# Performance work log

Measured on AMD Instinct MI355X. Metric: run time of the kernel, lower is better.

The kernel has to match this reference:

```python
import jax, jax.numpy as jnp
import numpy as np

FEAT = 128   # feat_dim == hidden_size
EDGE = 128   # edge_dim
H = FEAT
D = FEAT + EDGE          # TimeLSTM input size (att_dim)
SCALE = 5000000.0        # newAmazon time-decay divisor
B, L = 2048, 200


def setup_inputs() -> dict:
    key = jax.random.key(0)
    ks = jax.random.split(key, 12)
    seq = jax.random.normal(ks[0], (B, L, FEAT), jnp.float32)
    seq_e = jax.random.normal(ks[1], (B, L, EDGE), jnp.float32)
    # descending timestamps so time_span >= 0 (matches the module's assert)
    td = jax.random.randint(ks[2], (B, L), 0, 10_000_000)
    time_diff = jnp.flip(jnp.sort(td, axis=1), axis=1).astype(jnp.float32)
    src = jax.random.normal(ks[3], (B, FEAT), jnp.float32)
    src_t = jax.random.normal(ks[4], (B,), jnp.float32)
    seq_t = jax.random.normal(ks[5], (B, L), jnp.float32)
    mask = jnp.zeros((B, L), dtype=jnp.bool_)

    def lin(k, out_d, in_d):
        return (jax.random.normal(k, (out_d, in_d), jnp.float32)
                * np.float32(1.0 / np.sqrt(in_d)))

    # TimeLSTM params (W_all: h->4h, U_all: input->4h, W_d: h->h)
    W_all, b_W = lin(ks[6], 4 * H, H), jnp.zeros((4 * H,), jnp.float32)
    U_all, b_U = lin(ks[7], 4 * H, D), jnp.zeros((4 * H,), jnp.float32)
    W_d, b_d = lin(ks[8], H, H), jnp.zeros((H,), jnp.float32)
    # MergeLayer params
    fc1_w, fc1_b = lin(ks[9], FEAT, 2 * FEAT), jnp.zeros((FEAT,), jnp.float32)
    fc2_w, fc2_b = lin(ks[10], FEAT, FEAT), jnp.zeros((FEAT,), jnp.float32)
    return dict(src=src, src_t=src_t, seq=seq, seq_t=seq_t, seq_e=seq_e,
                time_diff=time_diff, mask=mask,
                W_all=W_all, b_W=b_W, U_all=U_all, b_U=b_U,
                W_d=W_d, b_d=b_d,
                fc1_w=fc1_w, fc1_b=fc1_b, fc2_w=fc2_w, fc2_b=fc2_b)


def reference(src, src_t, seq, seq_t, seq_e, time_diff, mask,
              W_all, b_W, U_all, b_U, W_d, b_d,
              fc1_w, fc1_b, fc2_w, fc2_b):
    # src_t, seq_t, mask are accepted but unused, matching the torch forward.
    seq_x = jnp.concatenate([seq, seq_e], axis=2)              # [B, L, D]
    # vectorized version of the python time-decay loop:
    # time_span[:, j] = (time_diff[:, j-1] - time_diff[:, j]) / SCALE, span[:,0]=0
    span = (time_diff[:, :-1] - time_diff[:, 1:]) / SCALE      # [B, L-1]
    time_span = jnp.concatenate(
        [jnp.zeros_like(time_diff[:, :1]), span], axis=1)      # [B, L]

    # batch the input projection over all timesteps in one GEMM
    u = jnp.einsum('bld,gd->blg', seq_x, U_all) + b_U          # [B, L, 4H]

    h0 = jnp.zeros((seq_x.shape[0], H), seq_x.dtype)
    c0 = jnp.zeros_like(h0)

    def step(carry, xs):
        h, c = carry
        u_t, t_t = xs                                          # [B,4H], [B]
        c_s1 = jnp.tanh(c @ W_d.T + b_d)                       # short-term mem
        c_adj = c - c_s1 + c_s1 * t_t[:, None]                 # time-decayed cell
        gates = h @ W_all.T + b_W + u_t
        f, i, o, g = jnp.split(gates, 4, axis=1)
        f = jax.nn.sigmoid(f)
        i = jax.nn.sigmoid(i)
        o = jax.nn.sigmoid(o)
        g = jax.nn.sigmoid(g)   # note: repo TimeLSTM uses sigmoid, not tanh
        c_new = f * c_adj + i * g
        h_new = o * jnp.tanh(c_new)
        return (h_new, c_new), h_new

    (hn, _cn), _outs = jax.lax.scan(
        step, (h0, c0), (jnp.swapaxes(u, 0, 1), time_span.T))  # scan over L

    # MergeLayer: fc2(relu(fc1(cat([hn, src]))))
    x = jnp.concatenate([hn, src], axis=1)                     # [B, 2*FEAT]
    hmid = jax.nn.relu(x @ fc1_w.T + fc1_b)
    return hmid @ fc2_w.T + fc2_b                              # [B, FEAT]
```

## Files before the change

kernel.cpp:

```cpp
#include <hip/hip_runtime.h>
#include <hip/hip_bf16.h>
#include <stdint.h>

#define L_ 200
#define SCALE_ 5000000.0f

typedef __attribute__((ext_vector_type(8))) short bf16x8;
typedef __attribute__((ext_vector_type(4))) float f32x4;

static __device__ __forceinline__ short to_bf16(float f) {
    __hip_bfloat16 h = __float2bfloat16(f);
    return *reinterpret_cast<short*>(&h);
}
static __device__ __forceinline__ float fsig(float x) {
    return __builtin_amdgcn_rcpf(1.0f + __builtin_amdgcn_exp2f(-1.442695041f * x));
}
static __device__ __forceinline__ float ftanh(float x) {
    return 1.0f - 2.0f * __builtin_amdgcn_rcpf(1.0f + __builtin_amdgcn_exp2f(2.885390082f * x));
}
static __device__ __forceinline__ float bf_lo(unsigned p) {
    union { unsigned u; float f; } c; c.u = p << 16; return c.f;
}
static __device__ __forceinline__ float bf_hi(unsigned p) {
    union { unsigned u; float f; } c; c.u = p & 0xffff0000u; return c.f;
}

__global__ void prep_kernel(const float* __restrict__ U_all, const float* __restrict__ W_all,
                            const float* __restrict__ W_d, const float* __restrict__ b_W,
                            const float* __restrict__ b_U, const float* __restrict__ b_d,
                            const float* __restrict__ time_diff,
                            short* __restrict__ ufrag, short* __restrict__ wfrag,
                            short* __restrict__ wdfrag, float* __restrict__ bias512,
                            float* __restrict__ bdo, float* __restrict__ tsw,
                            int n_total) {
    int i = blockIdx.x * 256 + threadIdx.x;
    if (i >= n_total) return;
    if (i < 131072) {
        int b = i & 7, lane = (i >> 3) & 63, kt = (i >> 9) & 7, g = (i >> 12) & 3, w = i >> 14;
        int n = g * 128 + w * 16 + (lane & 15);
        int k = kt * 32 + (lane >> 4) * 8 + b;
        ufrag[i] = to_bf16(U_all[n * 256 + k]);
    } else if (i < 196608) {
        int j = i - 131072;
        int b = j & 7, lane = (j >> 3) & 63, kt = (j >> 9) & 3, g = (j >> 11) & 3, w = j >> 13;
        int n = g * 128 + w * 16 + (lane & 15);
        int k = kt * 32 + (lane >> 4) * 8 + b;
        wfrag[j] = to_bf16(W_all[n * 128 + k]);
    } else if (i < 212992) {
        int m = i - 196608;
        int b = m & 7, lane = (m >> 3) & 63, kt = (m >> 9) & 3, w = m >> 11;
        int n = w * 16 + (lane & 15);
        int k = kt * 32 + (lane >> 4) * 8 + b;
        wdfrag[m] = to_bf16(W_d[n * 128 + k]);
    } else if (i < 213504) {
        int n = i - 212992;
        bias512[n] = b_W[n] + b_U[n];
    } else if (i < 213632) {
        int n = i - 213504;
        bdo[n] = b_d[n];
    } else {
        int j = i - 213632;
        int m = j & 15, rest = j >> 4;
        int l = rest % 200, g = rest / 200;
        float v = 0.0f;
        if (l > 0) {
            const float* td = time_diff + (size_t)(g * 16 + m) * L_;
            v = (td[l - 1] - td[l]) * (1.0f / SCALE_);
        }
        tsw[j] = v;
    }
}

__global__ __launch_bounds__(512, 2) void ugemm_kernel(
    const float* __restrict__ seq, const float* __restrict__ seq_e,
    const short* __restrict__ ufrag, short* __restrict__ uws) {
    __shared__ __align__(16) short aF[8192];

    const int tid = threadIdx.x;
    const int w = tid >> 6, lane = tid & 63;
    const int col16 = lane & 15, quad = lane >> 4;
    const int bid = blockIdx.x;
    const int g = bid & 127, lt = bid >> 7;

#pragma unroll
    for (int rep = 0; rep < 2; ++rep) {
        int id = rep * 512 + tid;
        int c = id & 31, m = id >> 5;
        int brow = m & 15, lloc = m >> 4;
        int k = c * 8;
        const float* srcp = (k < 128)
            ? seq   + ((size_t)(g * 16 + brow) * L_ + lt * 2 + lloc) * 128 + k
            : seq_e + ((size_t)(g * 16 + brow) * L_ + lt * 2 + lloc) * 128 + (k - 128);
        float4 p0 = ((const float4*)srcp)[0], p1 = ((const float4*)srcp)[1];
        bf16x8 sv;
        sv[0] = to_bf16(p0.x); sv[1] = to_bf16(p0.y); sv[2] = to_bf16(p0.z); sv[3] = to_bf16(p0.w);
        sv[4] = to_bf16(p1.x); sv[5] = to_bf16(p1.y); sv[6] = to_bf16(p1.z); sv[7] = to_bf16(p1.w);
        ((bf16x8*)aF)[(lloc * 8 + (c >> 2)) * 64 + (c & 3) * 16 + brow] = sv;
    }

    bf16x8 Bf[4][8];
#pragma unroll
    for (int j = 0; j < 4; ++j) {
        int nt = w * 4 + j, gg = nt >> 3, ww = nt & 7;
#pragma unroll
        for (int kt = 0; kt < 8; ++kt)
            Bf[j][kt] = ((const bf16x8*)ufrag)[(((ww * 4 + gg) * 8) + kt) * 64 + lane];
    }

    f32x4 acc[2][4];
#pragma unroll
    for (int mt = 0; mt < 2; ++mt)
#pragma unroll
        for (int j = 0; j < 4; ++j) acc[mt][j] = (f32x4){0.f, 0.f, 0.f, 0.f};

    __syncthreads();

#pragma unroll
    for (int kt = 0; kt < 8; ++kt) {
        bf16x8 a0 = ((const bf16x8*)aF)[(0 * 8 + kt) * 64 + lane];
        bf16x8 a1 = ((const bf16x8*)aF)[(1 * 8 + kt) * 64 + lane];
#pragma unroll
        for (int j = 0; j < 4; ++j) {
            acc[0][j] = __builtin_amdgcn_mfma_f32_16x16x32_bf16(a0, Bf[j][kt], acc[0][j], 0, 0, 0);
            acc[1][j] = __builtin_amdgcn_mfma_f32_16x16x32_bf16(a1, Bf[j][kt], acc[1][j], 0, 0, 0);
        }
    }

#pragma unroll
    for (int mt = 0; mt < 2; ++mt)
#pragma unroll
        for (int j = 0; j < 4; ++j) {
            int n = (w * 4 + j) * 16 + col16;
            size_t base = (((size_t)g * L_ + lt * 2 + mt) * 512 + n) * 16 + quad * 4;
            unsigned lo = (unsigned short)to_bf16(acc[mt][j][0])
                        | ((unsigned)(unsigned short)to_bf16(acc[mt][j][1]) << 16);
            unsigned hi = (unsigned short)to_bf16(acc[mt][j][2])
                        | ((unsigned)(unsigned short)to_bf16(acc[mt][j][3]) << 16);
            uint2 v; v.x = lo; v.y = hi;
            *(uint2*)(uws + base) = v;
        }
}

__global__ __launch_bounds__(512, 2) void rec_kernel(
    const short* __restrict__ uws, const short* __restrict__ wfrag,
    const short* __restrict__ wdfrag, const float* __restrict__ bias512,
    const float* __restrict__ bdv, const float* __restrict__ tsw,
    float* __restrict__ hn_buf) {

    __shared__ __align__(16) short hf[2][2048];
    __shared__ __align__(16) short cf[2][2048];

    const int tid = threadIdx.x;
    const int w = tid >> 6, lane = tid & 63;
    const int col16 = lane & 15, quad = lane >> 4;
    const int g = blockIdx.x;

    bf16x8 wB[4][4], wd[4];
#pragma unroll
    for (int gg = 0; gg < 4; ++gg)
#pragma unroll
        for (int kt = 0; kt < 4; ++kt)
            wB[gg][kt] = ((const bf16x8*)wfrag)[((w * 4 + gg) * 4 + kt) * 64 + lane];
#pragma unroll
    for (int kt = 0; kt < 4; ++kt)
        wd[kt] = ((const bf16x8*)wdfrag)[(w * 4 + kt) * 64 + lane];

    float bs[4];
#pragma unroll
    for (int gg = 0; gg < 4; ++gg) bs[gg] = bias512[gg * 128 + w * 16 + col16];
    const float bd = bdv[w * 16 + col16];

    for (int i = tid; i < 2048; i += 512) {
        hf[0][i] = 0; hf[1][i] = 0; cf[0][i] = 0; cf[1][i] = 0;
    }

    const int kto = (w >> 1) * 512 + ((w & 1) * 2 + (col16 >> 3)) * 128 + (col16 & 7);

    uint2 ucur[4], unxt[4];
#pragma unroll
    for (int gg = 0; gg < 4; ++gg)
        ucur[gg] = *(const uint2*)(uws + (((size_t)g * L_ + 0) * 512 + gg * 128 + w * 16 + col16) * 16 + quad * 4);
    float4 tcur = *(const float4*)(tsw + ((size_t)g * L_ + 0) * 16 + quad * 4);
    float4 tnxt;

    __syncthreads();

    f32x4 cacc = {0.f, 0.f, 0.f, 0.f};
    float hreg[4] = {0.f, 0.f, 0.f, 0.f};
    int par = 0;

    for (int t = 0; t < L_; ++t) {
        int tp = (t + 1 < L_) ? t + 1 : L_ - 1;
#pragma unroll
        for (int gg = 0; gg < 4; ++gg)
            unxt[gg] = *(const uint2*)(uws + (((size_t)g * L_ + tp) * 512 + gg * 128 + w * 16 + col16) * 16 + quad * 4);
        tnxt = *(const float4*)(tsw + ((size_t)g * L_ + tp) * 16 + quad * 4);

        f32x4 acc[4];
#pragma unroll
        for (int gg = 0; gg < 4; ++gg) {
            acc[gg][0] = bs[gg] + bf_lo(ucur[gg].x);
            acc[gg][1] = bs[gg] + bf_hi(ucur[gg].x);
            acc[gg][2] = bs[gg] + bf_lo(ucur[gg].y);
            acc[gg][3] = bs[gg] + bf_hi(ucur[gg].y);
        }
#pragma unroll
        for (int kt = 0; kt < 4; ++kt) {
            bf16x8 a = ((const bf16x8*)hf[par])[kt * 64 + lane];
#pragma unroll
            for (int gg = 0; gg < 4; ++gg)
                acc[gg] = __builtin_amdgcn_mfma_f32_16x16x32_bf16(a, wB[gg][kt], acc[gg], 0, 0, 0);
        }
        f32x4 cs = {bd, bd, bd, bd};
#pragma unroll
        for (int kt = 0; kt < 4; ++kt) {
            bf16x8 a = ((const bf16x8*)cf[par])[kt * 64 + lane];
            cs = __builtin_amdgcn_mfma_f32_16x16x32_bf16(a, wd[kt], cs, 0, 0, 0);
        }

#pragma unroll
        for (int r = 0; r < 4; ++r) {
            float ttv = (r == 0) ? tcur.x : (r == 1) ? tcur.y : (r == 2) ? tcur.z : tcur.w;
            float f   = fsig(acc[0][r]);
            float i_  = fsig(acc[1][r]);
            float o   = fsig(acc[2][r]);
            float g4  = fsig(acc[3][r]);
            float cs1 = ftanh(cs[r]);
            float ca  = cacc[r] - cs1 + cs1 * ttv;
            float cn  = f * ca + i_ * g4;
            float hv  = o * ftanh(cn);
            cacc[r] = cn;
            hreg[r] = hv;
            hf[par ^ 1][kto + (quad * 4 + r) * 8] = to_bf16(hv);
            cf[par ^ 1][kto + (quad * 4 + r) * 8] = to_bf16(cn);
        }
        __syncthreads();
#pragma unroll
        for (int gg = 0; gg < 4; ++gg) ucur[gg] = unxt[gg];
        tcur = tnxt;
        par ^= 1;
    }

#pragma unroll
    for (int r = 0; r < 4; ++r)
        hn_buf[(size_t)(g * 16 + quad * 4 + r) * 128 + w * 16 + col16] = hreg[r];
}

__global__ __launch_bounds__(512, 2) void lstm_kernel(
    const float* __restrict__ seq, const float* __restrict__ seq_e,
    const float* __restrict__ time_diff,
    const short* __restrict__ ufrag, const short* __restrict__ wfrag,
    const short* __restrict__ wdfrag, const float* __restrict__ bias512,
    const float* __restrict__ bdv, float* __restrict__ hn_buf) {

    __shared__ __align__(16) short xfrag[2][8][512];
    __shared__ __align__(16) short hS[16 * 136];
    __shared__ __align__(16) short cS[16 * 136];
    __shared__ float tspan[16 * 201];

    const int tid = threadIdx.x;
    const int w = tid >> 6, lane = tid & 63;
    const int col16 = lane & 15, quad = lane >> 4;
    const int row0 = quad * 4;
    const int b0 = blockIdx.x * 16;

    bf16x8 uB[4][8], wB[4][4], wd[4];
#pragma unroll
    for (int g = 0; g < 4; ++g)
#pragma unroll
        for (int kt = 0; kt < 8; ++kt)
            uB[g][kt] = ((const bf16x8*)ufrag)[((w * 4 + g) * 8 + kt) * 64 + lane];
#pragma unroll
    for (int g = 0; g < 4; ++g)
#pragma unroll
        for (int kt = 0; kt < 4; ++kt)
            wB[g][kt] = ((const bf16x8*)wfrag)[((w * 4 + g) * 4 + kt) * 64 + lane];
#pragma unroll
    for (int kt = 0; kt < 4; ++kt)
        wd[kt] = ((const bf16x8*)wdfrag)[(w * 4 + kt) * 64 + lane];

    float bs[4];
#pragma unroll
    for (int g = 0; g < 4; ++g) bs[g] = bias512[g * 128 + w * 16 + col16];
    const float bd = bdv[w * 16 + col16];

    for (int i = tid; i < 16 * L_; i += 512) {
        int r = i / L_, t = i - r * L_;
        float v = 0.0f;
        if (t > 0) {
            const float* td = time_diff + (size_t)(b0 + r) * L_;
            v = (td[t - 1] - td[t]) * (1.0f / SCALE_);
        }
        tspan[r * 201 + t] = v;
    }
    for (int i = tid; i < 16 * 136; i += 512) { hS[i] = 0; cS[i] = 0; }

    const int kb = w * 32 + quad * 8;
    const float* xsrc = (kb < 128)
        ? (seq   + (size_t)(b0 + col16) * L_ * 128 + kb)
        : (seq_e + (size_t)(b0 + col16) * L_ * 128 + (kb - 128));

    {
        const float4* p = (const float4*)xsrc;
        float4 a0 = p[0], a1 = p[1];
        bf16x8 sv;
        sv[0] = to_bf16(a0.x); sv[1] = to_bf16(a0.y); sv[2] = to_bf16(a0.z); sv[3] = to_bf16(a0.w);
        sv[4] = to_bf16(a1.x); sv[5] = to_bf16(a1.y); sv[6] = to_bf16(a1.z); sv[7] = to_bf16(a1.w);
        ((bf16x8*)xfrag[0][w])[lane] = sv;
    }
    __syncthreads();

    f32x4 cacc = {0.f, 0.f, 0.f, 0.f};
    float hreg[4] = {0.f, 0.f, 0.f, 0.f};
    int par = 0;

    for (int t = 0; t < L_; ++t) {
        int tt = (t + 1 < L_) ? (t + 1) : (L_ - 1);
        const float4* p = (const float4*)(xsrc + (size_t)tt * 128);
        float4 a0 = p[0], a1 = p[1];

        f32x4 acc[4];
#pragma unroll
        for (int g = 0; g < 4; ++g) acc[g] = (f32x4){bs[g], bs[g], bs[g], bs[g]};
#pragma unroll
        for (int kt = 0; kt < 8; ++kt) {
            bf16x8 a = ((const bf16x8*)xfrag[par][kt])[lane];
#pragma unroll
            for (int g = 0; g < 4; ++g)
                acc[g] = __builtin_amdgcn_mfma_f32_16x16x32_bf16(a, uB[g][kt], acc[g], 0, 0, 0);
        }
#pragma unroll
        for (int kt = 0; kt < 4; ++kt) {
            bf16x8 a = *(const bf16x8*)&hS[col16 * 136 + kt * 32 + quad * 8];
#pragma unroll
            for (int g = 0; g < 4; ++g)
                acc[g] = __builtin_amdgcn_mfma_f32_16x16x32_bf16(a, wB[g][kt], acc[g], 0, 0, 0);
        }
        f32x4 cs = {bd, bd, bd, bd};
#pragma unroll
        for (int kt = 0; kt < 4; ++kt) {
            bf16x8 a = *(const bf16x8*)&cS[col16 * 136 + kt * 32 + quad * 8];
            cs = __builtin_amdgcn_mfma_f32_16x16x32_bf16(a, wd[kt], cs, 0, 0, 0);
        }
        __syncthreads();

#pragma unroll
        for (int r = 0; r < 4; ++r) {
            float ttv = tspan[(row0 + r) * 201 + t];
            float f   = fsig(acc[0][r]);
            float i_  = fsig(acc[1][r]);
            float o   = fsig(acc[2][r]);
            float g4  = fsig(acc[3][r]);
            float cs1 = ftanh(cs[r]);
            float ca  = cacc[r] - cs1 + cs1 * ttv;
            float cn  = f * ca + i_ * g4;
            float hv  = o * ftanh(cn);
            cacc[r] = cn;
            hreg[r] = hv;
            hS[(row0 + r) * 136 + w * 16 + col16] = to_bf16(hv);
            cS[(row0 + r) * 136 + w * 16 + col16] = to_bf16(cn);
        }
        {
            bf16x8 sv;
            sv[0] = to_bf16(a0.x); sv[1] = to_bf16(a0.y); sv[2] = to_bf16(a0.z); sv[3] = to_bf16(a0.w);
            sv[4] = to_bf16(a1.x); sv[5] = to_bf16(a1.y); sv[6] = to_bf16(a1.z); sv[7] = to_bf16(a1.w);
            ((bf16x8*)xfrag[par ^ 1][w])[lane] = sv;
        }
        par ^= 1;
        __syncthreads();
    }

#pragma unroll
    for (int r = 0; r < 4; ++r)
        hn_buf[(size_t)(b0 + row0 + r) * 128 + w * 16 + col16] = hreg[r];
}

__global__ __launch_bounds__(256) void merge_kernel(
    const float* __restrict__ src, const float* __restrict__ fc1w,
    const float* __restrict__ fc1b, const float* __restrict__ fc2w,
    const float* __restrict__ fc2b, float* __restrict__ out) {
    __shared__ float xc[16][256];
    __shared__ float hm[16][128];
    const int tid = threadIdx.x;
    const int b0 = blockIdx.x * 16;
    for (int i = tid; i < 16 * 256; i += 256) {
        int r = i >> 8, k = i & 255;
        xc[r][k] = (k < 128) ? out[(size_t)(b0 + r) * 128 + k]
                             : src[(size_t)(b0 + r) * 128 + (k - 128)];
    }
    __syncthreads();
#pragma unroll
    for (int ii = 0; ii < 8; ++ii) {
        int o = tid + 256 * ii;
        int r = o >> 7, m = o & 127;
        const float4* wr = (const float4*)(fc1w + m * 256);
        const float4* xr = (const float4*)(xc[r]);
        float acc = fc1b[m];
        for (int k4 = 0; k4 < 64; ++k4) {
            float4 a = wr[k4], b = xr[k4];
            acc += a.x * b.x + a.y * b.y + a.z * b.z + a.w * b.w;
        }
        hm[r][m] = fmaxf(acc, 0.0f);
    }
    __syncthreads();
#pragma unroll
    for (int ii = 0; ii < 8; ++ii) {
        int o = tid + 256 * ii;
        int r = o >> 7, j = o & 127;
        const float4* wr = (const float4*)(fc2w + j * 128);
        const float4* xr = (const float4*)(hm[r]);
        float acc = fc2b[j];
        for (int k4 = 0; k4 < 32; ++k4) {
            float4 a = wr[k4], b = xr[k4];
            acc += a.x * b.x + a.y * b.y + a.z * b.z + a.w * b.w;
        }
        out[(size_t)(b0 + r) * 128 + j] = acc;
    }
}

extern "C" void kernel_launch(void* const* d_in, const int* in_sizes, int n_in,
                              void* d_out, int out_size, void* d_ws, size_t ws_size,
                              hipStream_t stream) {
    const float* src       = (const float*)d_in[0];
    const float* seq       = (const float*)d_in[2];
    const float* seq_e     = (const float*)d_in[4];
    const float* time_diff = (const float*)d_in[5];
    const float* W_all     = (const float*)d_in[7];
    const float* b_W       = (const float*)d_in[8];
    const float* U_all     = (const float*)d_in[9];
    const float* b_U       = (const float*)d_in[10];
    const float* W_d       = (const float*)d_in[11];
    const float* b_d       = (const float*)d_in[12];
    const float* fc1w      = (const float*)d_in[13];
    const float* fc1b      = (const float*)d_in[14];
    const float* fc2w      = (const float*)d_in[15];
    const float* fc2b      = (const float*)d_in[16];

    char* ws = (char*)d_ws;
    short* ufrag   = (short*)(ws);
    short* wfrag   = (short*)(ws + 262144);
    short* wdfrag  = (short*)(ws + 393216);
    float* bias512 = (float*)(ws + 425984);
    float* bdo     = (float*)(ws + 428032);
    float* tsw     = (float*)(ws + 430080);
    short* uws     = (short*)(ws + 2068480);
    float* outp    = (float*)d_out;

    const size_t NEED_SPLIT = 2068480ull + 419430400ull;
    const bool split = ws_size >= NEED_SPLIT;

    if (split) {
        prep_kernel<<<2435, 256, 0, stream>>>(U_all, W_all, W_d, b_W, b_U, b_d, time_diff,
                                              ufrag, wfrag, wdfrag, bias512, bdo, tsw, 623232);
        ugemm_kernel<<<12800, 512, 0, stream>>>(seq, seq_e, ufrag, uws);
        rec_kernel<<<128, 512, 0, stream>>>(uws, wfrag, wdfrag, bias512, bdo, tsw, outp);
    } else {
        prep_kernel<<<835, 256, 0, stream>>>(U_all, W_all, W_d, b_W, b_U, b_d, time_diff,
                                             ufrag, wfrag, wdfrag, bias512, bdo, tsw, 213632);
        lstm_kernel<<<128, 512, 0, stream>>>(seq, seq_e, time_diff,
                                             ufrag, wfrag, wdfrag, bias512, bdo, outp);
    }
    merge_kernel<<<128, 256, 0, stream>>>(src, fc1w, fc1b, fc2w, fc2b, outp);
}
```

Measured before the change: 1.020 ms.

## Persistent double-buffered U-GEMM and split recurrence across twice as many blocks

The input-projection GEMM kernel becomes persistent: each block keeps its U weight fragments in registers and loops over 10 time-pairs. It prefetches the next tile from global memory into a second LDS buffer while the current one runs, and uses an XOR swizzle on the LDS slots. The recurrence kernel now launches 256 blocks of 8 batch rows each instead of 128 blocks of 16, padding the MFMA M dimension so only half the quads write h/c. This doubles CU coverage for the latency-bound serial scan at the cost of wasted MFMA rows. U and time-span values are also prefetched two steps ahead instead of one.

```diff
diff --git a/kernel.cpp b/kernel.cpp
--- a/kernel.cpp
+++ b/kernel.cpp
@@ -74,71 +74,111 @@
 __global__ __launch_bounds__(512, 2) void ugemm_kernel(
     const float* __restrict__ seq, const float* __restrict__ seq_e,
     const short* __restrict__ ufrag, short* __restrict__ uws) {
-    __shared__ __align__(16) short aF[8192];
+    __shared__ __align__(16) short aF[2][8192];
 
     const int tid = threadIdx.x;
     const int w = tid >> 6, lane = tid & 63;
     const int col16 = lane & 15, quad = lane >> 4;
     const int bid = blockIdx.x;
-    const int g = bid & 127, lt = bid >> 7;
-
+    const int g = bid & 127;
+    const int ltc = bid >> 7;
+
+    bf16x8 Bf[4][8];
+#pragma unroll
+    for (int j = 0; j < 4; ++j) {
+        int nt = w * 4 + j, gg = nt >> 3, ww = nt & 7;
+#pragma unroll
+        for (int kt = 0; kt < 8; ++kt)
+            Bf[j][kt] = ((const bf16x8*)ufrag)[(((ww * 4 + gg) * 8) + kt) * 64 + lane];
+    }
+
+    const float* sp[2];
+    int sslot[2];
 #pragma unroll
     for (int rep = 0; rep < 2; ++rep) {
         int id = rep * 512 + tid;
         int c = id & 31, m = id >> 5;
         int brow = m & 15, lloc = m >> 4;
         int k = c * 8;
-        const float* srcp = (k < 128)
-            ? seq   + ((size_t)(g * 16 + brow) * L_ + lt * 2 + lloc) * 128 + k
-            : seq_e + ((size_t)(g * 16 + brow) * L_ + lt * 2 + lloc) * 128 + (k - 128);
-        float4 p0 = ((const float4*)srcp)[0], p1 = ((const float4*)srcp)[1];
+        sp[rep] = (k < 128)
+            ? seq   + ((size_t)(g * 16 + brow) * L_ + ltc * 20 + lloc) * 128 + k
+            : seq_e + ((size_t)(g * 16 + brow) * L_ + ltc * 20 + lloc) * 128 + (k - 128);
+        int s = (lloc * 8 + (c >> 2)) * 64 + (c & 3) * 16 + brow;
+        sslot[rep] = s ^ ((s >> 4) & 7);
+    }
+
+#pragma unroll
+    for (int rep = 0; rep < 2; ++rep) {
+        const float4* p = (const float4*)sp[rep];
+        float4 a = p[0], b = p[1];
         bf16x8 sv;
-        sv[0] = to_bf16(p0.x); sv[1] = to_bf16(p0.y); sv[2] = to_bf16(p0.z); sv[3] = to_bf16(p0.w);
-        sv[4] = to_bf16(p1.x); sv[5] = to_bf16(p1.y); sv[6] = to_bf16(p1.z); sv[7] = to_bf16(p1.w);
-        ((bf16x8*)aF)[(lloc * 8 + (c >> 2)) * 64 + (c & 3) * 16 + brow] = sv;
-    }
-
-    bf16x8 Bf[4][8];
-#pragma unroll
-    for (int j = 0; j < 4; ++j) {
-        int nt = w * 4 + j, gg = nt >> 3, ww = nt & 7;
-#pragma unroll
-        for (int kt = 0; kt < 8; ++kt)
-            Bf[j][kt] = ((const bf16x8*)ufrag)[(((ww * 4 + gg) * 8) + kt) * 64 + lane];
-    }
-
-    f32x4 acc[2][4];
-#pragma unroll
-    for (int mt = 0; mt < 2; ++mt)
-#pragma unroll
-        for (int j = 0; j < 4; ++j) acc[mt][j] = (f32x4){0.f, 0.f, 0.f, 0.f};
+        sv[0] = to_bf16(a.x); sv[1] = to_bf16(a.y); sv[2] = to_bf16(a.z); sv[3] = to_bf16(a.w);
+        sv[4] = to_bf16(b.x); sv[5] = to_bf16(b.y); sv[6] = to_bf16(b.z); sv[7] = to_bf16(b.w);
+        ((bf16x8*)aF[0])[sslot[rep]] = sv;
+    }
+
+    short* ub = uws + ((size_t)g * L_ + ltc * 20) * 8192
+              + ((size_t)(w * 4) * 16 + col16) * 16 + quad * 4;
 
     __syncthreads();
 
-#pragma unroll
-    for (int kt = 0; kt < 8; ++kt) {
-        bf16x8 a0 = ((const bf16x8*)aF)[(0 * 8 + kt) * 64 + lane];
-        bf16x8 a1 = ((const bf16x8*)aF)[(1 * 8 + kt) * 64 + lane];
-#pragma unroll
-        for (int j = 0; j < 4; ++j) {
-            acc[0][j] = __builtin_amdgcn_mfma_f32_16x16x32_bf16(a0, Bf[j][kt], acc[0][j], 0, 0, 0);
-            acc[1][j] = __builtin_amdgcn_mfma_f32_16x16x32_bf16(a1, Bf[j][kt], acc[1][j], 0, 0, 0);
-        }
-    }
-
-#pragma unroll
-    for (int mt = 0; mt < 2; ++mt)
-#pragma unroll
-        for (int j = 0; j < 4; ++j) {
-            int n = (w * 4 + j) * 16 + col16;
-            size_t base = (((size_t)g * L_ + lt * 2 + mt) * 512 + n) * 16 + quad * 4;
-            unsigned lo = (unsigned short)to_bf16(acc[mt][j][0])
-                        | ((unsigned)(unsigned short)to_bf16(acc[mt][j][1]) << 16);
-            unsigned hi = (unsigned short)to_bf16(acc[mt][j][2])
-                        | ((unsigned)(unsigned short)to_bf16(acc[mt][j][3]) << 16);
-            uint2 v; v.x = lo; v.y = hi;
-            *(uint2*)(uws + base) = v;
-        }
+    int par = 0;
+#pragma unroll 2
+    for (int it = 0; it < 10; ++it) {
+        float4 nA[2], nB[2];
+        if (it < 9) {
+#pragma unroll
+            for (int rep = 0; rep < 2; ++rep) {
+                const float4* p = (const float4*)(sp[rep] + (it + 1) * 256);
+                nA[rep] = p[0]; nB[rep] = p[1];
+            }
+        }
+
+        f32x4 acc[2][4];
+#pragma unroll
+        for (int mt = 0; mt < 2; ++mt)
+#pragma unroll
+            for (int j = 0; j < 4; ++j) acc[mt][j] = (f32x4){0.f, 0.f, 0.f, 0.f};
+
+#pragma unroll
+        for (int kt = 0; kt < 8; ++kt) {
+            int s0 = kt * 64 + lane;
+            int s1 = 512 + kt * 64 + lane;
+            bf16x8 a0 = ((const bf16x8*)aF[par])[s0 ^ ((s0 >> 4) & 7)];
+            bf16x8 a1 = ((const bf16x8*)aF[par])[s1 ^ ((s1 >> 4) & 7)];
+#pragma unroll
+            for (int j = 0; j < 4; ++j) {
+                acc[0][j] = __builtin_amdgcn_mfma_f32_16x16x32_bf16(a0, Bf[j][kt], acc[0][j], 0, 0, 0);
+                acc[1][j] = __builtin_amdgcn_mfma_f32_16x16x32_bf16(a1, Bf[j][kt], acc[1][j], 0, 0, 0);
+            }
+        }
+
+#pragma unroll
+        for (int mt = 0; mt < 2; ++mt)
+#pragma unroll
+            for (int j = 0; j < 4; ++j) {
+                unsigned lo = (unsigned short)to_bf16(acc[mt][j][0])
+                            | ((unsigned)(unsigned short)to_bf16(acc[mt][j][1]) << 16);
+                unsigned hi = (unsigned short)to_bf16(acc[mt][j][2])
+                            | ((unsigned)(unsigned short)to_bf16(acc[mt][j][3]) << 16);
+                uint2 v; v.x = lo; v.y = hi;
+                *(uint2*)(ub + (size_t)it * 16384 + mt * 8192 + j * 256) = v;
+            }
+
+        if (it < 9) {
+#pragma unroll
+            for (int rep = 0; rep < 2; ++rep) {
+                bf16x8 sv;
+                sv[0] = to_bf16(nA[rep].x); sv[1] = to_bf16(nA[rep].y);
+                sv[2] = to_bf16(nA[rep].z); sv[3] = to_bf16(nA[rep].w);
+                sv[4] = to_bf16(nB[rep].x); sv[5] = to_bf16(nB[rep].y);
+                sv[6] = to_bf16(nB[rep].z); sv[7] = to_bf16(nB[rep].w);
+                ((bf16x8*)aF[par ^ 1])[sslot[rep]] = sv;
+            }
+        }
+        __syncthreads();
+        par ^= 1;
+    }
 }
 
 __global__ __launch_bounds__(512, 2) void rec_kernel(
@@ -154,6 +194,7 @@
     const int w = tid >> 6, lane = tid & 63;
     const int col16 = lane & 15, quad = lane >> 4;
     const int g = blockIdx.x;
+    const int sub = ((g & 1) * 8) + ((quad & 1) * 4);
 
     bf16x8 wB[4][4], wd[4];
 #pragma unroll
@@ -176,12 +217,18 @@
 
     const int kto = (w >> 1) * 512 + ((w & 1) * 2 + (col16 >> 3)) * 128 + (col16 & 7);
 
-    uint2 ucur[4], unxt[4];
-#pragma unroll
-    for (int gg = 0; gg < 4; ++gg)
-        ucur[gg] = *(const uint2*)(uws + (((size_t)g * L_ + 0) * 512 + gg * 128 + w * 16 + col16) * 16 + quad * 4);
-    float4 tcur = *(const float4*)(tsw + ((size_t)g * L_ + 0) * 16 + quad * 4);
-    float4 tnxt;
+    const short* uptr = uws + (size_t)(g >> 1) * ((size_t)L_ * 8192)
+                      + (w * 16 + col16) * 16 + sub;
+    const float* tptr = tsw + (size_t)(g >> 1) * (L_ * 16) + sub;
+
+    uint2 u0[4], u1[4], u2[4];
+    float4 tv0, tv1, tv2;
+#pragma unroll
+    for (int gg = 0; gg < 4; ++gg) u0[gg] = *(const uint2*)(uptr + gg * 2048);
+    tv0 = *(const float4*)tptr;
+#pragma unroll
+    for (int gg = 0; gg < 4; ++gg) u1[gg] = *(const uint2*)(uptr + 8192 + gg * 2048);
+    tv1 = *(const float4*)(tptr + 16);
 
     __syncthreads();
 
@@ -190,19 +237,19 @@
     int par = 0;
 
     for (int t = 0; t < L_; ++t) {
-        int tp = (t + 1 < L_) ? t + 1 : L_ - 1;
+        int t2 = (t + 2 < L_) ? t + 2 : L_ - 1;
 #pragma unroll
         for (int gg = 0; gg < 4; ++gg)
-            unxt[gg] = *(const uint2*)(uws + (((size_t)g * L_ + tp) * 512 + gg * 128 + w * 16 + col16) * 16 + quad * 4);
-        tnxt = *(const float4*)(tsw + ((size_t)g * L_ + tp) * 16 + quad * 4);
+            u2[gg] = *(const uint2*)(uptr + (size_t)t2 * 8192 + gg * 2048);
+        tv2 = *(const float4*)(tptr + (size_t)t2 * 16);
 
         f32x4 acc[4];
 #pragma unroll
         for (int gg = 0; gg < 4; ++gg) {
-            acc[gg][0] = bs[gg] + bf_lo(ucur[gg].x);
-            acc[gg][1] = bs[gg] + bf_hi(ucur[gg].x);
-            acc[gg][2] = bs[gg] + bf_lo(ucur[gg].y);
-            acc[gg][3] = bs[gg] + bf_hi(ucur[gg].y);
+            acc[gg][0] = bs[gg] + bf_lo(u0[gg].x);
+            acc[gg][1] = bs[gg] + bf_hi(u0[gg].x);
+            acc[gg][2] = bs[gg] + bf_lo(u0[gg].y);
+            acc[gg][3] = bs[gg] + bf_hi(u0[gg].y);
         }
 #pragma unroll
         for (int kt = 0; kt < 4; ++kt) {
@@ -220,7 +267,7 @@
 
 #pragma unroll
         for (int r = 0; r < 4; ++r) {
-            float ttv = (r == 0) ? tcur.x : (r == 1) ? tcur.y : (r == 2) ? tcur.z : tcur.w;
+            float ttv = (r == 0) ? tv0.x : (r == 1) ? tv0.y : (r == 2) ? tv0.z : tv0.w;
             float f   = fsig(acc[0][r]);
             float i_  = fsig(acc[1][r]);
             float o   = fsig(acc[2][r]);
@@ -231,19 +278,23 @@
             float hv  = o * ftanh(cn);
             cacc[r] = cn;
             hreg[r] = hv;
-            hf[par ^ 1][kto + (quad * 4 + r) * 8] = to_bf16(hv);
-            cf[par ^ 1][kto + (quad * 4 + r) * 8] = to_bf16(cn);
+            if (quad < 2) {
+                hf[par ^ 1][kto + (quad * 4 + r) * 8] = to_bf16(hv);
+                cf[par ^ 1][kto + (quad * 4 + r) * 8] = to_bf16(cn);
+            }
         }
         __syncthreads();
 #pragma unroll
-        for (int gg = 0; gg < 4; ++gg) ucur[gg] = unxt[gg];
-        tcur = tnxt;
+        for (int gg = 0; gg < 4; ++gg) { u0[gg] = u1[gg]; u1[gg] = u2[gg]; }
+        tv0 = tv1; tv1 = tv2;
         par ^= 1;
     }
 
-#pragma unroll
-    for (int r = 0; r < 4; ++r)
-        hn_buf[(size_t)(g * 16 + quad * 4 + r) * 128 + w * 16 + col16] = hreg[r];
+    if (quad < 2) {
+#pragma unroll
+        for (int r = 0; r < 4; ++r)
+            hn_buf[(size_t)(g * 8 + quad * 4 + r) * 128 + w * 16 + col16] = hreg[r];
+    }
 }
 
 __global__ __launch_bounds__(512, 2) void lstm_kernel(
@@ -452,8 +503,8 @@
     if (split) {
         prep_kernel<<<2435, 256, 0, stream>>>(U_all, W_all, W_d, b_W, b_U, b_d, time_diff,
                                               ufrag, wfrag, wdfrag, bias512, bdo, tsw, 623232);
-        ugemm_kernel<<<12800, 512, 0, stream>>>(seq, seq_e, ufrag, uws);
-        rec_kernel<<<128, 512, 0, stream>>>(uws, wfrag, wdfrag, bias512, bdo, tsw, outp);
+        ugemm_kernel<<<1280, 512, 0, stream>>>(seq, seq_e, ufrag, uws);
+        rec_kernel<<<256, 512, 0, stream>>>(uws, wfrag, wdfrag, bias512, bdo, tsw, outp);
     } else {
         prep_kernel<<<835, 256, 0, stream>>>(U_all, W_all, W_d, b_W, b_U, b_d, time_diff,
                                              ufrag, wfrag, wdfrag, bias512, bdo, tsw, 213632);
```

Result: faster. 958.3 us (-6.1%).

## Drop split GEMM path; fuse input projection into recurrent kernel with single barrier

Applied to the files above, without the earlier changes.

Removes the separate U-projection GEMM kernel, which wrote a large bf16 workspace, along with the recurrence kernel that read it back. The fused LSTM kernel now always runs and computes the input projection per timestep from seq/seq_e. The recurrent h/c state now uses double-buffered MFMA-fragment layouts, which removes one __syncthreads per step. This cuts hundreds of MB of global traffic, but the input-projection MFMAs now sit on the serial critical path of only 128 blocks.

```diff
diff --git a/kernel.cpp b/kernel.cpp
--- a/kernel.cpp
+++ b/kernel.cpp
@@ -18,21 +18,13 @@
 static __device__ __forceinline__ float ftanh(float x) {
     return 1.0f - 2.0f * __builtin_amdgcn_rcpf(1.0f + __builtin_amdgcn_exp2f(2.885390082f * x));
 }
-static __device__ __forceinline__ float bf_lo(unsigned p) {
-    union { unsigned u; float f; } c; c.u = p << 16; return c.f;
-}
-static __device__ __forceinline__ float bf_hi(unsigned p) {
-    union { unsigned u; float f; } c; c.u = p & 0xffff0000u; return c.f;
-}
 
 __global__ void prep_kernel(const float* __restrict__ U_all, const float* __restrict__ W_all,
                             const float* __restrict__ W_d, const float* __restrict__ b_W,
                             const float* __restrict__ b_U, const float* __restrict__ b_d,
-                            const float* __restrict__ time_diff,
                             short* __restrict__ ufrag, short* __restrict__ wfrag,
                             short* __restrict__ wdfrag, float* __restrict__ bias512,
-                            float* __restrict__ bdo, float* __restrict__ tsw,
-                            int n_total) {
+                            float* __restrict__ bdo, int n_total) {
     int i = blockIdx.x * 256 + threadIdx.x;
     if (i >= n_total) return;
     if (i < 131072) {
@@ -55,207 +47,22 @@
     } else if (i < 213504) {
         int n = i - 212992;
         bias512[n] = b_W[n] + b_U[n];
-    } else if (i < 213632) {
+    } else {
         int n = i - 213504;
         bdo[n] = b_d[n];
-    } else {
-        int j = i - 213632;
-        int m = j & 15, rest = j >> 4;
-        int l = rest % 200, g = rest / 200;
-        float v = 0.0f;
-        if (l > 0) {
-            const float* td = time_diff + (size_t)(g * 16 + m) * L_;
-            v = (td[l - 1] - td[l]) * (1.0f / SCALE_);
-        }
-        tsw[j] = v;
-    }
-}
-
-__global__ __launch_bounds__(512, 2) void ugemm_kernel(
-    const float* __restrict__ seq, const float* __restrict__ seq_e,
-    const short* __restrict__ ufrag, short* __restrict__ uws) {
-    __shared__ __align__(16) short aF[8192];
-
-    const int tid = threadIdx.x;
-    const int w = tid >> 6, lane = tid & 63;
-    const int col16 = lane & 15, quad = lane >> 4;
-    const int bid = blockIdx.x;
-    const int g = bid & 127, lt = bid >> 7;
-
-#pragma unroll
-    for (int rep = 0; rep < 2; ++rep) {
-        int id = rep * 512 + tid;
-        int c = id & 31, m = id >> 5;
-        int brow = m & 15, lloc = m >> 4;
-        int k = c * 8;
-        const float* srcp = (k < 128)
-            ? seq   + ((size_t)(g * 16 + brow) * L_ + lt * 2 + lloc) * 128 + k
-            : seq_e + ((size_t)(g * 16 + brow) * L_ + lt * 2 + lloc) * 128 + (k - 128);
-        float4 p0 = ((const float4*)srcp)[0], p1 = ((const float4*)srcp)[1];
-        bf16x8 sv;
-        sv[0] = to_bf16(p0.x); sv[1] = to_bf16(p0.y); sv[2] = to_bf16(p0.z); sv[3] = to_bf16(p0.w);
-        sv[4] = to_bf16(p1.x); sv[5] = to_bf16(p1.y); sv[6] = to_bf16(p1.z); sv[7] = to_bf16(p1.w);
-        ((bf16x8*)aF)[(lloc * 8 + (c >> 2)) * 64 + (c & 3) * 16 + brow] = sv;
-    }
-
-    bf16x8 Bf[4][8];
-#pragma unroll
-    for (int j = 0; j < 4; ++j) {
-        int nt = w * 4 + j, gg = nt >> 3, ww = nt & 7;
-#pragma unroll
-        for (int kt = 0; kt < 8; ++kt)
-            Bf[j][kt] = ((const bf16x8*)ufrag)[(((ww * 4 + gg) * 8) + kt) * 64 + lane];
-    }
-
-    f32x4 acc[2][4];
-#pragma unroll
-    for (int mt = 0; mt < 2; ++mt)
-#pragma unroll
-        for (int j = 0; j < 4; ++j) acc[mt][j] = (f32x4){0.f, 0.f, 0.f, 0.f};
-
-    __syncthreads();
-
-#pragma unroll
-    for (int kt = 0; kt < 8; ++kt) {
-        bf16x8 a0 = ((const bf16x8*)aF)[(0 * 8 + kt) * 64 + lane];
-        bf16x8 a1 = ((const bf16x8*)aF)[(1 * 8 + kt) * 64 + lane];
-#pragma unroll
-        for (int j = 0; j < 4; ++j) {
-            acc[0][j] = __builtin_amdgcn_mfma_f32_16x16x32_bf16(a0, Bf[j][kt], acc[0][j], 0, 0, 0);
-            acc[1][j] = __builtin_amdgcn_mfma_f32_16x16x32_bf16(a1, Bf[j][kt], acc[1][j], 0, 0, 0);
-        }
-    }
-
-#pragma unroll
-    for (int mt = 0; mt < 2; ++mt)
-#pragma unroll
-        for (int j = 0; j < 4; ++j) {
-            int n = (w * 4 + j) * 16 + col16;
-            size_t base = (((size_t)g * L_ + lt * 2 + mt) * 512 + n) * 16 + quad * 4;
-            unsigned lo = (unsigned short)to_bf16(acc[mt][j][0])
-                        | ((unsigned)(unsigned short)to_bf16(acc[mt][j][1]) << 16);
-            unsigned hi = (unsigned short)to_bf16(acc[mt][j][2])
-                        | ((unsigned)(unsigned short)to_bf16(acc[mt][j][3]) << 16);
-            uint2 v; v.x = lo; v.y = hi;
-            *(uint2*)(uws + base) = v;
-        }
-}
-
-__global__ __launch_bounds__(512, 2) void rec_kernel(
-    const short* __restrict__ uws, const short* __restrict__ wfrag,
-    const short* __restrict__ wdfrag, const float* __restrict__ bias512,
-    const float* __restrict__ bdv, const float* __restrict__ tsw,
-    float* __restrict__ hn_buf) {
-
-    __shared__ __align__(16) short hf[2][2048];
-    __shared__ __align__(16) short cf[2][2048];
-
-    const int tid = threadIdx.x;
-    const int w = tid >> 6, lane = tid & 63;
-    const int col16 = lane & 15, quad = lane >> 4;
-    const int g = blockIdx.x;
-
-    bf16x8 wB[4][4], wd[4];
-#pragma unroll
-    for (int gg = 0; gg < 4; ++gg)
-#pragma unroll
-        for (int kt = 0; kt < 4; ++kt)
-            wB[gg][kt] = ((const bf16x8*)wfrag)[((w * 4 + gg) * 4 + kt) * 64 + lane];
-#pragma unroll
-    for (int kt = 0; kt < 4; ++kt)
-        wd[kt] = ((const bf16x8*)wdfrag)[(w * 4 + kt) * 64 + lane];
-
-    float bs[4];
-#pragma unroll
-    for (int gg = 0; gg < 4; ++gg) bs[gg] = bias512[gg * 128 + w * 16 + col16];
-    const float bd = bdv[w * 16 + col16];
-
-    for (int i = tid; i < 2048; i += 512) {
-        hf[0][i] = 0; hf[1][i] = 0; cf[0][i] = 0; cf[1][i] = 0;
-    }
-
-    const int kto = (w >> 1) * 512 + ((w & 1) * 2 + (col16 >> 3)) * 128 + (col16 & 7);
-
-    uint2 ucur[4], unxt[4];
-#pragma unroll
-    for (int gg = 0; gg < 4; ++gg)
-        ucur[gg] = *(const uint2*)(uws + (((size_t)g * L_ + 0) * 512 + gg * 128 + w * 16 + col16) * 16 + quad * 4);
-    float4 tcur = *(const float4*)(tsw + ((size_t)g * L_ + 0) * 16 + quad * 4);
-    float4 tnxt;
-
-    __syncthreads();
-
-    f32x4 cacc = {0.f, 0.f, 0.f, 0.f};
-    float hreg[4] = {0.f, 0.f, 0.f, 0.f};
-    int par = 0;
-
-    for (int t = 0; t < L_; ++t) {
-        int tp = (t + 1 < L_) ? t + 1 : L_ - 1;
-#pragma unroll
-        for (int gg = 0; gg < 4; ++gg)
-            unxt[gg] = *(const uint2*)(uws + (((size_t)g * L_ + tp) * 512 + gg * 128 + w * 16 + col16) * 16 + quad * 4);
-        tnxt = *(const float4*)(tsw + ((size_t)g * L_ + tp) * 16 + quad * 4);
-
-        f32x4 acc[4];
-#pragma unroll
-        for (int gg = 0; gg < 4; ++gg) {
-            acc[gg][0] = bs[gg] + bf_lo(ucur[gg].x);
-            acc[gg][1] = bs[gg] + bf_hi(ucur[gg].x);
-            acc[gg][2] = bs[gg] + bf_lo(ucur[gg].y);
-            acc[gg][3] = bs[gg] + bf_hi(ucur[gg].y);
-        }
-#pragma unroll
-        for (int kt = 0; kt < 4; ++kt) {
-            bf16x8 a = ((const bf16x8*)hf[par])[kt * 64 + lane];
-#pragma unroll
-            for (int gg = 0; gg < 4; ++gg)
-                acc[gg] = __builtin_amdgcn_mfma_f32_16x16x32_bf16(a, wB[gg][kt], acc[gg], 0, 0, 0);
-        }
-        f32x4 cs = {bd, bd, bd, bd};
-#pragma unroll
-        for (int kt = 0; kt < 4; ++kt) {
-            bf16x8 a = ((const bf16x8*)cf[par])[kt * 64 + lane];
-            cs = __builtin_amdgcn_mfma_f32_16x16x32_bf16(a, wd[kt], cs, 0, 0, 0);
-        }
-
-#pragma unroll
-        for (int r = 0; r < 4; ++r) {
-            float ttv = (r == 0) ? tcur.x : (r == 1) ? tcur.y : (r == 2) ? tcur.z : tcur.w;
-            float f   = fsig(acc[0][r]);
-            float i_  = fsig(acc[1][r]);
-            float o   = fsig(acc[2][r]);
-            float g4  = fsig(acc[3][r]);
-            float cs1 = ftanh(cs[r]);
-            float ca  = cacc[r] - cs1 + cs1 * ttv;
-            float cn  = f * ca + i_ * g4;
-            float hv  = o * ftanh(cn);
-            cacc[r] = cn;
-            hreg[r] = hv;
-            hf[par ^ 1][kto + (quad * 4 + r) * 8] = to_bf16(hv);
-            cf[par ^ 1][kto + (quad * 4 + r) * 8] = to_bf16(cn);
-        }
-        __syncthreads();
-#pragma unroll
-        for (int gg = 0; gg < 4; ++gg) ucur[gg] = unxt[gg];
-        tcur = tnxt;
-        par ^= 1;
-    }
-
-#pragma unroll
-    for (int r = 0; r < 4; ++r)
-        hn_buf[(size_t)(g * 16 + quad * 4 + r) * 128 + w * 16 + col16] = hreg[r];
-}
-
-__global__ __launch_bounds__(512, 2) void lstm_kernel(
+    }
+}
+
+__global__ __launch_bounds__(512, 2) void fused_kernel(
     const float* __restrict__ seq, const float* __restrict__ seq_e,
     const float* __restrict__ time_diff,
     const short* __restrict__ ufrag, const short* __restrict__ wfrag,
     const short* __restrict__ wdfrag, const float* __restrict__ bias512,
     const float* __restrict__ bdv, float* __restrict__ hn_buf) {
 
-    __shared__ __align__(16) short xfrag[2][8][512];
-    __shared__ __align__(16) short hS[16 * 136];
-    __shared__ __align__(16) short cS[16 * 136];
+    __shared__ __align__(16) short xf[2][8][512];
+    __shared__ __align__(16) short hf[2][2048];
+    __shared__ __align__(16) short cf[2][2048];
     __shared__ float tspan[16 * 201];
 
     const int tid = threadIdx.x;
@@ -293,7 +100,11 @@
         }
         tspan[r * 201 + t] = v;
     }
-    for (int i = tid; i < 16 * 136; i += 512) { hS[i] = 0; cS[i] = 0; }
+    for (int i = tid; i < 2048; i += 512) {
+        hf[0][i] = 0; hf[1][i] = 0; cf[0][i] = 0; cf[1][i] = 0;
+    }
+
+    const int kto = (w >> 1) * 512 + ((w & 1) * 2 + (col16 >> 3)) * 128 + (col16 & 7);
 
     const int kb = w * 32 + quad * 8;
     const float* xsrc = (kb < 128)
@@ -306,7 +117,7 @@
         bf16x8 sv;
         sv[0] = to_bf16(a0.x); sv[1] = to_bf16(a0.y); sv[2] = to_bf16(a0.z); sv[3] = to_bf16(a0.w);
         sv[4] = to_bf16(a1.x); sv[5] = to_bf16(a1.y); sv[6] = to_bf16(a1.z); sv[7] = to_bf16(a1.w);
-        ((bf16x8*)xfrag[0][w])[lane] = sv;
+        ((bf16x8*)xf[0][w])[lane] = sv;
     }
     __syncthreads();
 
@@ -317,21 +128,21 @@
     for (int t = 0; t < L_; ++t) {
         int tt = (t + 1 < L_) ? (t + 1) : (L_ - 1);
         const float4* p = (const float4*)(xsrc + (size_t)tt * 128);
-        float4 a0 = p[0], a1 = p[1];
+        float4 nx0 = p[0], nx1 = p[1];
 
         f32x4 acc[4];
 #pragma unroll
         for (int g = 0; g < 4; ++g) acc[g] = (f32x4){bs[g], bs[g], bs[g], bs[g]};
 #pragma unroll
         for (int kt = 0; kt < 8; ++kt) {
-            bf16x8 a = ((const bf16x8*)xfrag[par][kt])[lane];
+            bf16x8 a = ((const bf16x8*)xf[par][kt])[lane];
 #pragma unroll
             for (int g = 0; g < 4; ++g)
                 acc[g] = __builtin_amdgcn_mfma_f32_16x16x32_bf16(a, uB[g][kt], acc[g], 0, 0, 0);
         }
 #pragma unroll
         for (int kt = 0; kt < 4; ++kt) {
-            bf16x8 a = *(const bf16x8*)&hS[col16 * 136 + kt * 32 + quad * 8];
+            bf16x8 a = ((const bf16x8*)hf[par])[kt * 64 + lane];
 #pragma unroll
             for (int g = 0; g < 4; ++g)
                 acc[g] = __builtin_amdgcn_mfma_f32_16x16x32_bf16(a, wB[g][kt], acc[g], 0, 0, 0);
@@ -339,10 +150,9 @@
         f32x4 cs = {bd, bd, bd, bd};
 #pragma unroll
         for (int kt = 0; kt < 4; ++kt) {
-            bf16x8 a = *(const bf16x8*)&cS[col16 * 136 + kt * 32 + quad * 8];
+            bf16x8 a = ((const bf16x8*)cf[par])[kt * 64 + lane];
             cs = __builtin_amdgcn_mfma_f32_16x16x32_bf16(a, wd[kt], cs, 0, 0, 0);
         }
-        __syncthreads();
 
 #pragma unroll
         for (int r = 0; r < 4; ++r) {
@@ -357,17 +167,17 @@
             float hv  = o * ftanh(cn);
             cacc[r] = cn;
             hreg[r] = hv;
-            hS[(row0 + r) * 136 + w * 16 + col16] = to_bf16(hv);
-            cS[(row0 + r) * 136 + w * 16 + col16] = to_bf16(cn);
+            hf[par ^ 1][kto + (row0 + r) * 8] = to_bf16(hv);
+            cf[par ^ 1][kto + (row0 + r) * 8] = to_bf16(cn);
         }
         {
             bf16x8 sv;
-            sv[0] = to_bf16(a0.x); sv[1] = to_bf16(a0.y); sv[2] = to_bf16(a0.z); sv[3] = to_bf16(a0.w);
-            sv[4] = to_bf16(a1.x); sv[5] = to_bf16(a1.y); sv[6] = to_bf16(a1.z); sv[7] = to_bf16(a1.w);
-            ((bf16x8*)xfrag[par ^ 1][w])[lane] = sv;
-        }
+            sv[0] = to_bf16(nx0.x); sv[1] = to_bf16(nx0.y); sv[2] = to_bf16(nx0.z); sv[3] = to_bf16(nx0.w);
+            sv[4] = to_bf16(nx1.x); sv[5] = to_bf16(nx1.y); sv[6] = to_bf16(nx1.z); sv[7] = to_bf16(nx1.w);
+            ((bf16x8*)xf[par ^ 1][w])[lane] = sv;
+        }
+        __syncthreads();
         par ^= 1;
-        __syncthreads();
     }
 
 #pragma unroll
@@ -442,23 +252,11 @@
     short* wdfrag  = (short*)(ws + 393216);
     float* bias512 = (float*)(ws + 425984);
     float* bdo     = (float*)(ws + 428032);
-    float* tsw     = (float*)(ws + 430080);
-    short* uws     = (short*)(ws + 2068480);
     float* outp    = (float*)d_out;
 
-    const size_t NEED_SPLIT = 2068480ull + 419430400ull;
-    const bool split = ws_size >= NEED_SPLIT;
-
-    if (split) {
-        prep_kernel<<<2435, 256, 0, stream>>>(U_all, W_all, W_d, b_W, b_U, b_d, time_diff,
-                                              ufrag, wfrag, wdfrag, bias512, bdo, tsw, 623232);
-        ugemm_kernel<<<12800, 512, 0, stream>>>(seq, seq_e, ufrag, uws);
-        rec_kernel<<<128, 512, 0, stream>>>(uws, wfrag, wdfrag, bias512, bdo, tsw, outp);
-    } else {
-        prep_kernel<<<835, 256, 0, stream>>>(U_all, W_all, W_d, b_W, b_U, b_d, time_diff,
-                                             ufrag, wfrag, wdfrag, bias512, bdo, tsw, 213632);
-        lstm_kernel<<<128, 512, 0, stream>>>(seq, seq_e, time_diff,
-                                             ufrag, wfrag, wdfrag, bias512, bdo, outp);
-    }
+    prep_kernel<<<835, 256, 0, stream>>>(U_all, W_all, W_d, b_W, b_U, b_d,
+                                         ufrag, wfrag, wdfrag, bias512, bdo, 213632);
+    fused_kernel<<<128, 512, 0, stream>>>(seq, seq_e, time_diff,
+                                          ufrag, wfrag, wdfrag, bias512, bdo, outp);
     merge_kernel<<<128, 256, 0, stream>>>(src, fc1w, fc1b, fc2w, fc2b, outp);
 }
```

Measured after the change: 1.178 ms. +15.5%, slower.
